# Performance work log

Hardware: AMD Instinct MI355X
Metric: run time of the kernel (lower is better)

## Reference

```python
import jax, jax.numpy as jnp
import numpy as np

N, C, W = 64, 64, 4096
F, WW = 64, 9

def next_power2(n):
    return int(2 ** np.ceil(np.log2(n)))

def setup_inputs() -> dict:
    key = jax.random.key(0)
    k1, k2, k3 = jax.random.split(key, 3)
    x = jax.random.normal(k1, (N, C, W), dtype=jnp.float32)
    filt = jax.random.normal(k2, (F, C, WW), dtype=jnp.float32)
    bias = jax.random.normal(k3, (F,), dtype=jnp.float32)
    return {"x": x, "filt": filt, "bias": bias}

def reference(x, filt, bias):
    # FFT-based valid cross-correlation, no spectral compression
    # (preserve_energy_rate=None, index_back=None, out_size=None, padding=None).
    n_, c_, w_ = x.shape
    f_, _, ww_ = filt.shape
    out_W = w_ - ww_ + 1  # valid correlation output length
    fftsize = next_power2(w_ + ww_ - 1)
    xf = jnp.fft.rfft(x, n=fftsize)            # [N, C, K] complex64
    wf = jnp.fft.rfft(filt, n=fftsize)         # [F, C, K] complex64
    # correlation = ifft(Xf * conj(Wf)); sum over channels in freq domain
    of = jnp.einsum('nck,fck->nfk', xf, jnp.conj(wf))  # [N, F, K]
    out = jnp.fft.irfft(of, n=fftsize)[..., :out_W]    # [N, F, out_W] float32
    # original adds bias[f] once per channel iteration -> C * bias
    out = out + (c_ * bias)[None, :, None]
    return out
```

## Files before the change

kernel.cpp:

```cpp
#include <hip/hip_runtime.h>
#include <stdint.h>

#define N_   64
#define C_   64
#define W_   4096
#define F_   64
#define WW_  9
#define OW_  4088
#define WBLK 128
#define WROWS 136
#define TILES 2
#define STRIPES 16

typedef __bf16 bf16x8 __attribute__((ext_vector_type(8)));
typedef float  f32x4  __attribute__((ext_vector_type(4)));

__device__ __forceinline__ unsigned short f2bf(float f) {
    union { float f; uint32_t u; } v; v.f = f;
    uint32_t u = v.u;
    return (unsigned short)((u + 0x7FFFu + ((u >> 16) & 1u)) >> 16);
}

__global__ __launch_bounds__(256) void prep_filt_k(const float* __restrict__ filt,
                                                   unsigned short* __restrict__ filtB) {
    int id = blockIdx.x * 256 + threadIdx.x;
    if (id < WW_ * F_ * C_) {
        int j    = id & 7;
        int lane = (id >> 3) & 63;
        int u    = (id >> 9) & 1;
        int m    = (id >> 10) & 1;
        int f0h  = (id >> 11) & 1;
        int t    = id >> 12;
        int l15  = lane & 15, lg = lane >> 4;
        int f = f0h * 32 + u * 16 + l15;
        int c = m * 32 + lg * 8 + j;
        filtB[id] = f2bf(filt[(f * C_ + c) * WW_ + t]);
    }
}

__global__ __launch_bounds__(256, 3) void conv_k(const float* __restrict__ x,
                                                 const unsigned short* __restrict__ filtB,
                                                 const float* __restrict__ bias,
                                                 float* __restrict__ out) {
    __shared__ unsigned short xs[2][WROWS * 64];

    const int tid   = threadIdx.x;
    const int lane  = tid & 63;
    const int wv    = tid >> 6;
    const int n     = blockIdx.y;
    const int wbase = blockIdx.x * (TILES * WBLK);
    const int f0h   = wv & 1;
    const int whb   = (wv >> 1) * 64;
    const int l15   = lane & 15;
    const int lg    = lane >> 4;

    const int sc0 = tid >> 5;
    const int sw  = (tid & 31) << 2;
    const int hc  = tid >> 1;
    const int hwo = 128 + (tid & 1) * 4;

    const float* xrow = x + ((size_t)(n * C_ + sc0)) * W_;
    const unsigned short* Bb = filtB + f0h * 2048 + lane * 8;

    const float bv0 = 64.0f * bias[f0h * 32 + l15];
    const float bv1 = 64.0f * bias[f0h * 32 + 16 + l15];

    float4 r[8];
    float4 rh;

    auto LOADS = [&](int w0) {
        #pragma unroll
        for (int i = 0; i < 8; ++i)
            r[i] = *reinterpret_cast<const float4*>(xrow + (size_t)i * 8 * W_ + w0 + sw);
        if (tid < 128) {
            int hw = w0 + hwo;
            if (hw < W_) rh = *reinterpret_cast<const float4*>(x + ((size_t)(n * C_ + hc)) * W_ + hw);
            else         rh = (float4){0.f, 0.f, 0.f, 0.f};
        }
    };

    auto WRITE = [&](int b) {
        unsigned short* dst = xs[b];
        #pragma unroll
        for (int i = 0; i < 8; ++i) {
            const float* rp = &r[i].x;
            #pragma unroll
            for (int j = 0; j < 4; ++j) {
                int w = sw + j;
                dst[w * 64 + (((i ^ (w & 7)) << 3) | sc0)] = f2bf(rp[j]);
            }
        }
        if (tid < 128) {
            int cg = hc >> 3, cs = hc & 7;
            const float* rp = &rh.x;
            #pragma unroll
            for (int j = 0; j < 4; ++j) {
                int w = hwo + j;
                dst[w * 64 + (((cg ^ (w & 7)) << 3) | cs)] = f2bf(rp[j]);
            }
        }
    };

    auto COMPUTE = [&](int b, int w0) {
        const unsigned short* src = xs[b];
        f32x4 acc[4][2];
        #pragma unroll
        for (int s = 0; s < 4; ++s) {
            acc[s][0] = (f32x4){0.f, 0.f, 0.f, 0.f};
            acc[s][1] = (f32x4){0.f, 0.f, 0.f, 0.f};
        }
        bf16x8 Bc[4], Bn[4];
        #pragma unroll
        for (int q = 0; q < 4; ++q)
            Bc[q] = *reinterpret_cast<const bf16x8*>(Bb + (q >> 1) * 1024 + (q & 1) * 512);
        #pragma unroll
        for (int t = 0; t < WW_; ++t) {
            if (t < WW_ - 1) {
                #pragma unroll
                for (int q = 0; q < 4; ++q)
                    Bn[q] = *reinterpret_cast<const bf16x8*>(Bb + (t + 1) * 4096 + (q >> 1) * 1024 + (q & 1) * 512);
            }
            #pragma unroll
            for (int m = 0; m < 2; ++m) {
                #pragma unroll
                for (int s = 0; s < 4; ++s) {
                    int row   = whb + s * 16 + l15 + t;
                    int chunk = ((m << 2) | lg) ^ (row & 7);
                    bf16x8 a  = *reinterpret_cast<const bf16x8*>(&src[row * 64 + chunk * 8]);
                    acc[s][0] = __builtin_amdgcn_mfma_f32_16x16x32_bf16(a, Bc[m * 2 + 0], acc[s][0], 0, 0, 0);
                    acc[s][1] = __builtin_amdgcn_mfma_f32_16x16x32_bf16(a, Bc[m * 2 + 1], acc[s][1], 0, 0, 0);
                }
            }
            if (t < WW_ - 1) {
                #pragma unroll
                for (int q = 0; q < 4; ++q) Bc[q] = Bn[q];
            }
        }
        const int fb = f0h * 32 + l15;
        #pragma unroll
        for (int s = 0; s < 4; ++s) {
            int wg = w0 + whb + s * 16 + lg * 4;
            if (wg < OW_) {
                float4 o0, o1;
                o0.x = acc[s][0][0] + bv0; o0.y = acc[s][0][1] + bv0;
                o0.z = acc[s][0][2] + bv0; o0.w = acc[s][0][3] + bv0;
                o1.x = acc[s][1][0] + bv1; o1.y = acc[s][1][1] + bv1;
                o1.z = acc[s][1][2] + bv1; o1.w = acc[s][1][3] + bv1;
                *reinterpret_cast<float4*>(out + ((size_t)(n * F_ + fb) * OW_ + wg))      = o0;
                *reinterpret_cast<float4*>(out + ((size_t)(n * F_ + fb + 16) * OW_ + wg)) = o1;
            }
        }
    };

    LOADS(wbase);
    WRITE(0);
    LOADS(wbase + WBLK);
    __syncthreads();
    COMPUTE(0, wbase);
    WRITE(1);
    __syncthreads();
    COMPUTE(1, wbase + WBLK);
}

extern "C" void kernel_launch(void* const* d_in, const int* in_sizes, int n_in,
                              void* d_out, int out_size, void* d_ws, size_t ws_size,
                              hipStream_t stream) {
    const float* x    = (const float*)d_in[0];
    const float* filt = (const float*)d_in[1];
    const float* bias = (const float*)d_in[2];
    float* out        = (float*)d_out;

    unsigned short* filtB = (unsigned short*)d_ws;

    prep_filt_k<<<(WW_ * F_ * C_ + 255) / 256, 256, 0, stream>>>(filt, filtB);

    dim3 grid(STRIPES, N_);
    conv_k<<<grid, 256, 0, stream>>>(x, filtB, bias, out);
}
```

Before: 55.00 us.

## Use one tile per block with vectorized 4-channel bf16 LDS staging

Drops the two-tile software pipeline (double-buffered LDS, loads of the next tile overlapped with compute) in favour of one 128-wide tile per block, which doubles the grid to 32x64 blocks and halves LDS per block. Staging now loads float4s from four channels and writes packed ushort4 bf16 values into the swizzled LDS layout, replacing scalar 2-byte stores. Launch bounds rise to 4 blocks per CU to get more occupancy. The cost is losing the load/compute overlap inside a block and doing the halo load with scalar strided global reads.

```diff
diff --git a/kernel.cpp b/kernel.cpp
--- a/kernel.cpp
+++ b/kernel.cpp
@@ -9,8 +9,6 @@
 #define OW_  4088
 #define WBLK 128
 #define WROWS 136
-#define TILES 2
-#define STRIPES 16
 
 typedef __bf16 bf16x8 __attribute__((ext_vector_type(8)));
 typedef float  f32x4  __attribute__((ext_vector_type(4)));
@@ -38,128 +36,126 @@
     }
 }
 
-__global__ __launch_bounds__(256, 3) void conv_k(const float* __restrict__ x,
+__global__ __launch_bounds__(256, 4) void conv_k(const float* __restrict__ x,
                                                  const unsigned short* __restrict__ filtB,
                                                  const float* __restrict__ bias,
                                                  float* __restrict__ out) {
-    __shared__ unsigned short xs[2][WROWS * 64];
+    __shared__ unsigned short xs[WROWS * 64];
 
-    const int tid   = threadIdx.x;
-    const int lane  = tid & 63;
-    const int wv    = tid >> 6;
-    const int n     = blockIdx.y;
-    const int wbase = blockIdx.x * (TILES * WBLK);
-    const int f0h   = wv & 1;
-    const int whb   = (wv >> 1) * 64;
-    const int l15   = lane & 15;
-    const int lg    = lane >> 4;
+    const int tid  = threadIdx.x;
+    const int lane = tid & 63;
+    const int wv   = tid >> 6;
+    const int n    = blockIdx.y;
+    const int w0   = blockIdx.x * WBLK;
 
-    const int sc0 = tid >> 5;
-    const int sw  = (tid & 31) << 2;
-    const int hc  = tid >> 1;
-    const int hwo = 128 + (tid & 1) * 4;
+    {
+        const int c4 = (wv << 4) + (((tid >> 4) & 3) << 2);
+        const int wq = (tid & 15) << 2;
+        const int cg = c4 >> 3;
+        const int cs = c4 & 7;
+        const float* xb = x + ((size_t)(n * C_ + c4)) * W_ + w0;
+        #pragma unroll
+        for (int j = 0; j < 2; ++j) {
+            const int wl = wq + j * 64;
+            float4 r0 = *reinterpret_cast<const float4*>(xb + 0 * W_ + wl);
+            float4 r1 = *reinterpret_cast<const float4*>(xb + 1 * W_ + wl);
+            float4 r2 = *reinterpret_cast<const float4*>(xb + 2 * W_ + wl);
+            float4 r3 = *reinterpret_cast<const float4*>(xb + 3 * W_ + wl);
+            const float* p0 = &r0.x; const float* p1 = &r1.x;
+            const float* p2 = &r2.x; const float* p3 = &r3.x;
+            #pragma unroll
+            for (int jj = 0; jj < 4; ++jj) {
+                int w = wl + jj;
+                ushort4 u;
+                u.x = f2bf(p0[jj]); u.y = f2bf(p1[jj]);
+                u.z = f2bf(p2[jj]); u.w = f2bf(p3[jj]);
+                *reinterpret_cast<ushort4*>(&xs[w * 64 + ((cg ^ (w & 7)) << 3) + cs]) = u;
+            }
+        }
+        if (tid < 32) {
+            const int hc4 = (tid & 15) << 2;
+            const int hwl = 128 + ((tid >> 4) << 2);
+            const int hcg = hc4 >> 3;
+            const int hcs = hc4 & 7;
+            #pragma unroll
+            for (int jj = 0; jj < 4; ++jj) {
+                int w  = hwl + jj;
+                int gw = w0 + w;
+                ushort4 u;
+                if (gw < W_) {
+                    const float* hp = x + ((size_t)(n * C_ + hc4)) * W_ + gw;
+                    u.x = f2bf(hp[0]);
+                    u.y = f2bf(hp[(size_t)W_]);
+                    u.z = f2bf(hp[(size_t)2 * W_]);
+                    u.w = f2bf(hp[(size_t)3 * W_]);
+                } else {
+                    u.x = u.y = u.z = u.w = 0;
+                }
+                *reinterpret_cast<ushort4*>(&xs[w * 64 + ((hcg ^ (w & 7)) << 3) + hcs]) = u;
+            }
+        }
+    }
+    __syncthreads();
 
-    const float* xrow = x + ((size_t)(n * C_ + sc0)) * W_;
+    const int f0h = wv & 1;
+    const int whb = (wv >> 1) * 64;
+    const int l15 = lane & 15;
+    const int lg  = lane >> 4;
+
     const unsigned short* Bb = filtB + f0h * 2048 + lane * 8;
-
     const float bv0 = 64.0f * bias[f0h * 32 + l15];
     const float bv1 = 64.0f * bias[f0h * 32 + 16 + l15];
 
-    float4 r[8];
-    float4 rh;
+    f32x4 acc[4][2];
+    #pragma unroll
+    for (int s = 0; s < 4; ++s) {
+        acc[s][0] = (f32x4){0.f, 0.f, 0.f, 0.f};
+        acc[s][1] = (f32x4){0.f, 0.f, 0.f, 0.f};
+    }
 
-    auto LOADS = [&](int w0) {
+    bf16x8 Bc[4], Bn[4];
+    #pragma unroll
+    for (int q = 0; q < 4; ++q)
+        Bc[q] = *reinterpret_cast<const bf16x8*>(Bb + (q >> 1) * 1024 + (q & 1) * 512);
+
+    #pragma unroll
+    for (int t = 0; t < WW_; ++t) {
+        if (t < WW_ - 1) {
+            #pragma unroll
+            for (int q = 0; q < 4; ++q)
+                Bn[q] = *reinterpret_cast<const bf16x8*>(Bb + (t + 1) * 4096 + (q >> 1) * 1024 + (q & 1) * 512);
+        }
         #pragma unroll
-        for (int i = 0; i < 8; ++i)
-            r[i] = *reinterpret_cast<const float4*>(xrow + (size_t)i * 8 * W_ + w0 + sw);
-        if (tid < 128) {
-            int hw = w0 + hwo;
-            if (hw < W_) rh = *reinterpret_cast<const float4*>(x + ((size_t)(n * C_ + hc)) * W_ + hw);
-            else         rh = (float4){0.f, 0.f, 0.f, 0.f};
-        }
-    };
-
-    auto WRITE = [&](int b) {
-        unsigned short* dst = xs[b];
-        #pragma unroll
-        for (int i = 0; i < 8; ++i) {
-            const float* rp = &r[i].x;
+        for (int m = 0; m < 2; ++m) {
             #pragma unroll
-            for (int j = 0; j < 4; ++j) {
-                int w = sw + j;
-                dst[w * 64 + (((i ^ (w & 7)) << 3) | sc0)] = f2bf(rp[j]);
+            for (int s = 0; s < 4; ++s) {
+                int row   = whb + s * 16 + l15 + t;
+                int chunk = ((m << 2) | lg) ^ (row & 7);
+                bf16x8 a  = *reinterpret_cast<const bf16x8*>(&xs[row * 64 + chunk * 8]);
+                acc[s][0] = __builtin_amdgcn_mfma_f32_16x16x32_bf16(a, Bc[m * 2 + 0], acc[s][0], 0, 0, 0);
+                acc[s][1] = __builtin_amdgcn_mfma_f32_16x16x32_bf16(a, Bc[m * 2 + 1], acc[s][1], 0, 0, 0);
             }
         }
-        if (tid < 128) {
-            int cg = hc >> 3, cs = hc & 7;
-            const float* rp = &rh.x;
+        if (t < WW_ - 1) {
             #pragma unroll
-            for (int j = 0; j < 4; ++j) {
-                int w = hwo + j;
-                dst[w * 64 + (((cg ^ (w & 7)) << 3) | cs)] = f2bf(rp[j]);
-            }
+            for (int q = 0; q < 4; ++q) Bc[q] = Bn[q];
         }
-    };
+    }
 
-    auto COMPUTE = [&](int b, int w0) {
-        const unsigned short* src = xs[b];
-        f32x4 acc[4][2];
-        #pragma unroll
-        for (int s = 0; s < 4; ++s) {
-            acc[s][0] = (f32x4){0.f, 0.f, 0.f, 0.f};
-            acc[s][1] = (f32x4){0.f, 0.f, 0.f, 0.f};
+    const int fb = f0h * 32 + l15;
+    #pragma unroll
+    for (int s = 0; s < 4; ++s) {
+        int wg = w0 + whb + s * 16 + lg * 4;
+        if (wg < OW_) {
+            float4 o0, o1;
+            o0.x = acc[s][0][0] + bv0; o0.y = acc[s][0][1] + bv0;
+            o0.z = acc[s][0][2] + bv0; o0.w = acc[s][0][3] + bv0;
+            o1.x = acc[s][1][0] + bv1; o1.y = acc[s][1][1] + bv1;
+            o1.z = acc[s][1][2] + bv1; o1.w = acc[s][1][3] + bv1;
+            *reinterpret_cast<float4*>(out + ((size_t)(n * F_ + fb) * OW_ + wg))      = o0;
+            *reinterpret_cast<float4*>(out + ((size_t)(n * F_ + fb + 16) * OW_ + wg)) = o1;
         }
-        bf16x8 Bc[4], Bn[4];
-        #pragma unroll
-        for (int q = 0; q < 4; ++q)
-            Bc[q] = *reinterpret_cast<const bf16x8*>(Bb + (q >> 1) * 1024 + (q & 1) * 512);
-        #pragma unroll
-        for (int t = 0; t < WW_; ++t) {
-            if (t < WW_ - 1) {
-                #pragma unroll
-                for (int q = 0; q < 4; ++q)
-                    Bn[q] = *reinterpret_cast<const bf16x8*>(Bb + (t + 1) * 4096 + (q >> 1) * 1024 + (q & 1) * 512);
-            }
-            #pragma unroll
-            for (int m = 0; m < 2; ++m) {
-                #pragma unroll
-                for (int s = 0; s < 4; ++s) {
-                    int row   = whb + s * 16 + l15 + t;
-                    int chunk = ((m << 2) | lg) ^ (row & 7);
-                    bf16x8 a  = *reinterpret_cast<const bf16x8*>(&src[row * 64 + chunk * 8]);
-                    acc[s][0] = __builtin_amdgcn_mfma_f32_16x16x32_bf16(a, Bc[m * 2 + 0], acc[s][0], 0, 0, 0);
-                    acc[s][1] = __builtin_amdgcn_mfma_f32_16x16x32_bf16(a, Bc[m * 2 + 1], acc[s][1], 0, 0, 0);
-                }
-            }
-            if (t < WW_ - 1) {
-                #pragma unroll
-                for (int q = 0; q < 4; ++q) Bc[q] = Bn[q];
-            }
-        }
-        const int fb = f0h * 32 + l15;
-        #pragma unroll
-        for (int s = 0; s < 4; ++s) {
-            int wg = w0 + whb + s * 16 + lg * 4;
-            if (wg < OW_) {
-                float4 o0, o1;
-                o0.x = acc[s][0][0] + bv0; o0.y = acc[s][0][1] + bv0;
-                o0.z = acc[s][0][2] + bv0; o0.w = acc[s][0][3] + bv0;
-                o1.x = acc[s][1][0] + bv1; o1.y = acc[s][1][1] + bv1;
-                o1.z = acc[s][1][2] + bv1; o1.w = acc[s][1][3] + bv1;
-                *reinterpret_cast<float4*>(out + ((size_t)(n * F_ + fb) * OW_ + wg))      = o0;
-                *reinterpret_cast<float4*>(out + ((size_t)(n * F_ + fb + 16) * OW_ + wg)) = o1;
-            }
-        }
-    };
-
-    LOADS(wbase);
-    WRITE(0);
-    LOADS(wbase + WBLK);
-    __syncthreads();
-    COMPUTE(0, wbase);
-    WRITE(1);
-    __syncthreads();
-    COMPUTE(1, wbase + WBLK);
+    }
 }
 
 extern "C" void kernel_launch(void* const* d_in, const int* in_sizes, int n_in,
@@ -174,6 +170,6 @@
 
     prep_filt_k<<<(WW_ * F_ * C_ + 255) / 256, 256, 0, stream>>>(filt, filtB);
 
-    dim3 grid(STRIPES, N_);
+    dim3 grid(W_ / WBLK, N_);
     conv_k<<<grid, 256, 0, stream>>>(x, filtB, bias, out);
 }
```

After: 44.05 us. -19.9%, faster.

## Repack x staging to 4-channel packed bf16 LDS stores and drop filter prefetch

Applied to the files above, without the earlier changes.

Changes how each thread loads the input tile: each thread now reads 4 adjacent channels over 2×4 width positions instead of 8 channels with stride 8. It converts them with packed v_cvt_pk_bf16_f32 and writes 8-byte LDS stores instead of scalar 2-byte stores. The double-buffered filter register prefetch is replaced by loading the filter fragments just in time, and launch bounds are raised to 4 blocks per CU. This aims to cut LDS store instruction count and conversion cost and to free registers for occupancy, at the risk of exposing filter load latency inside the MFMA loop.

```diff
diff --git a/kernel.cpp b/kernel.cpp
--- a/kernel.cpp
+++ b/kernel.cpp
@@ -9,8 +9,6 @@
 #define OW_  4088
 #define WBLK 128
 #define WROWS 136
-#define TILES 2
-#define STRIPES 16
 
 typedef __bf16 bf16x8 __attribute__((ext_vector_type(8)));
 typedef float  f32x4  __attribute__((ext_vector_type(4)));
@@ -19,6 +17,13 @@
     union { float f; uint32_t u; } v; v.f = f;
     uint32_t u = v.u;
     return (unsigned short)((u + 0x7FFFu + ((u >> 16) & 1u)) >> 16);
+}
+
+__device__ __forceinline__ uint2 pk4(float a, float b, float c, float d) {
+    uint2 r;
+    asm volatile("v_cvt_pk_bf16_f32 %0, %1, %2" : "=v"(r.x) : "v"(a), "v"(b));
+    asm volatile("v_cvt_pk_bf16_f32 %0, %1, %2" : "=v"(r.y) : "v"(c), "v"(d));
+    return r;
 }
 
 __global__ __launch_bounds__(256) void prep_filt_k(const float* __restrict__ filt,
@@ -38,7 +43,7 @@
     }
 }
 
-__global__ __launch_bounds__(256, 3) void conv_k(const float* __restrict__ x,
+__global__ __launch_bounds__(256, 4) void conv_k(const float* __restrict__ x,
                                                  const unsigned short* __restrict__ filtB,
                                                  const float* __restrict__ bias,
                                                  float* __restrict__ out) {
@@ -48,33 +53,31 @@
     const int lane  = tid & 63;
     const int wv    = tid >> 6;
     const int n     = blockIdx.y;
-    const int wbase = blockIdx.x * (TILES * WBLK);
-    const int f0h   = wv & 1;
-    const int whb   = (wv >> 1) * 64;
-    const int l15   = lane & 15;
-    const int lg    = lane >> 4;
+    const int wbase = blockIdx.x * (2 * WBLK);
 
-    const int sc0 = tid >> 5;
-    const int sw  = (tid & 31) << 2;
-    const int hc  = tid >> 1;
-    const int hwo = 128 + (tid & 1) * 4;
+    const int c4 = (wv << 4) + (((tid >> 4) & 3) << 2);
+    const int wq = (tid & 15) << 2;
+    const int cg = c4 >> 3;
+    const int cs = c4 & 7;
+    const float* xb = x + ((size_t)(n * C_ + c4)) * W_;
+    const int hcw = tid >> 1;
+    const int hwq = 128 + ((tid & 1) << 2);
+    const int hcg = hcw >> 3;
+    const int hcs = hcw & 7;
+    const float* hb = x + ((size_t)(n * C_ + hcw)) * W_;
 
-    const float* xrow = x + ((size_t)(n * C_ + sc0)) * W_;
-    const unsigned short* Bb = filtB + f0h * 2048 + lane * 8;
-
-    const float bv0 = 64.0f * bias[f0h * 32 + l15];
-    const float bv1 = 64.0f * bias[f0h * 32 + 16 + l15];
-
-    float4 r[8];
+    float4 r[2][4];
     float4 rh;
 
     auto LOADS = [&](int w0) {
         #pragma unroll
-        for (int i = 0; i < 8; ++i)
-            r[i] = *reinterpret_cast<const float4*>(xrow + (size_t)i * 8 * W_ + w0 + sw);
+        for (int j = 0; j < 2; ++j)
+            #pragma unroll
+            for (int k = 0; k < 4; ++k)
+                r[j][k] = *reinterpret_cast<const float4*>(xb + (size_t)k * W_ + w0 + wq + j * 64);
         if (tid < 128) {
-            int hw = w0 + hwo;
-            if (hw < W_) rh = *reinterpret_cast<const float4*>(x + ((size_t)(n * C_ + hc)) * W_ + hw);
+            int gw = w0 + hwq;
+            if (gw < W_) rh = *reinterpret_cast<const float4*>(hb + gw);
             else         rh = (float4){0.f, 0.f, 0.f, 0.f};
         }
     };
@@ -82,24 +85,31 @@
     auto WRITE = [&](int b) {
         unsigned short* dst = xs[b];
         #pragma unroll
-        for (int i = 0; i < 8; ++i) {
-            const float* rp = &r[i].x;
+        for (int j = 0; j < 2; ++j) {
             #pragma unroll
-            for (int j = 0; j < 4; ++j) {
-                int w = sw + j;
-                dst[w * 64 + (((i ^ (w & 7)) << 3) | sc0)] = f2bf(rp[j]);
+            for (int jj = 0; jj < 4; ++jj) {
+                int w = wq + j * 64 + jj;
+                uint2 u2 = pk4((&r[j][0].x)[jj], (&r[j][1].x)[jj],
+                               (&r[j][2].x)[jj], (&r[j][3].x)[jj]);
+                *reinterpret_cast<uint2*>(&dst[w * 64 + ((cg ^ (w & 7)) << 3) + cs]) = u2;
             }
         }
         if (tid < 128) {
-            int cg = hc >> 3, cs = hc & 7;
-            const float* rp = &rh.x;
             #pragma unroll
-            for (int j = 0; j < 4; ++j) {
-                int w = hwo + j;
-                dst[w * 64 + (((cg ^ (w & 7)) << 3) | cs)] = f2bf(rp[j]);
+            for (int jj = 0; jj < 4; ++jj) {
+                int w = hwq + jj;
+                dst[w * 64 + ((hcg ^ (w & 7)) << 3) + hcs] = f2bf((&rh.x)[jj]);
             }
         }
     };
+
+    const int f0h = wv & 1;
+    const int whb = (wv >> 1) * 64;
+    const int l15 = lane & 15;
+    const int lg  = lane >> 4;
+    const unsigned short* Bb = filtB + f0h * 2048 + lane * 8;
+    const float bv0 = 64.0f * bias[f0h * 32 + l15];
+    const float bv1 = 64.0f * bias[f0h * 32 + 16 + l15];
 
     auto COMPUTE = [&](int b, int w0) {
         const unsigned short* src = xs[b];
@@ -109,31 +119,20 @@
             acc[s][0] = (f32x4){0.f, 0.f, 0.f, 0.f};
             acc[s][1] = (f32x4){0.f, 0.f, 0.f, 0.f};
         }
-        bf16x8 Bc[4], Bn[4];
-        #pragma unroll
-        for (int q = 0; q < 4; ++q)
-            Bc[q] = *reinterpret_cast<const bf16x8*>(Bb + (q >> 1) * 1024 + (q & 1) * 512);
         #pragma unroll
         for (int t = 0; t < WW_; ++t) {
-            if (t < WW_ - 1) {
-                #pragma unroll
-                for (int q = 0; q < 4; ++q)
-                    Bn[q] = *reinterpret_cast<const bf16x8*>(Bb + (t + 1) * 4096 + (q >> 1) * 1024 + (q & 1) * 512);
-            }
             #pragma unroll
             for (int m = 0; m < 2; ++m) {
+                bf16x8 b0 = *reinterpret_cast<const bf16x8*>(Bb + t * 4096 + m * 1024);
+                bf16x8 b1 = *reinterpret_cast<const bf16x8*>(Bb + t * 4096 + m * 1024 + 512);
                 #pragma unroll
                 for (int s = 0; s < 4; ++s) {
                     int row   = whb + s * 16 + l15 + t;
                     int chunk = ((m << 2) | lg) ^ (row & 7);
                     bf16x8 a  = *reinterpret_cast<const bf16x8*>(&src[row * 64 + chunk * 8]);
-                    acc[s][0] = __builtin_amdgcn_mfma_f32_16x16x32_bf16(a, Bc[m * 2 + 0], acc[s][0], 0, 0, 0);
-                    acc[s][1] = __builtin_amdgcn_mfma_f32_16x16x32_bf16(a, Bc[m * 2 + 1], acc[s][1], 0, 0, 0);
+                    acc[s][0] = __builtin_amdgcn_mfma_f32_16x16x32_bf16(a, b0, acc[s][0], 0, 0, 0);
+                    acc[s][1] = __builtin_amdgcn_mfma_f32_16x16x32_bf16(a, b1, acc[s][1], 0, 0, 0);
                 }
-            }
-            if (t < WW_ - 1) {
-                #pragma unroll
-                for (int q = 0; q < 4; ++q) Bc[q] = Bn[q];
             }
         }
         const int fb = f0h * 32 + l15;
@@ -174,6 +173,6 @@
 
     prep_filt_k<<<(WW_ * F_ * C_ + 255) / 256, 256, 0, stream>>>(filt, filtB);
 
-    dim3 grid(STRIPES, N_);
+    dim3 grid(W_ / (2 * WBLK), N_);
     conv_k<<<grid, 256, 0, stream>>>(x, filtB, bias, out);
 }
```

After: 48.09 us. 12.6% less time.
